# Kernel tuning notes

Measured on AMD Instinct MI355X. Metric: run time of the kernel, lower is better.

Reference implementation:

```python
import jax, jax.numpy as jnp
import numpy as np

TAU = 0.07
K = 50
EPS = 1e-8


def _flat_norm(x):
    # [B, C, H, W] -> [B*H*W, C], L2-normalized along C
    B, C = x.shape[0], x.shape[1]
    x = jnp.moveaxis(x, 1, -1).reshape(-1, C)
    n = jnp.linalg.norm(x, axis=-1, keepdims=True)
    return x / jnp.maximum(n, 1e-12)


def setup_inputs() -> dict:
    key = jax.random.key(0)
    ks = jax.random.split(key, 5)
    shp = (2, 128, 64, 64)
    lshp = (2, 4, 64, 64)
    return {
        "input": jax.random.normal(ks[0], shp, dtype=jnp.float32),
        "positive": jax.random.normal(ks[1], shp, dtype=jnp.float32),
        "negative": jax.random.normal(ks[2], shp, dtype=jnp.float32),
        "input_logits": jax.random.normal(ks[3], lshp, dtype=jnp.float32),
        "negative_logits": jax.random.normal(ks[4], lshp, dtype=jnp.float32),
    }


def reference(input, positive, negative, input_logits, negative_logits):
    norm_input = _flat_norm(input)        # [N, C]
    norm_positive = _flat_norm(positive)  # [N, C]
    norm_negative = _flat_norm(negative)  # [N, C]

    # check_input: multi-class logits branch (softmax over class dim, then max)
    in_probs = jax.nn.softmax(input_logits, axis=1)
    neg_probs = jax.nn.softmax(negative_logits, axis=1)
    seg_input = jnp.argmax(in_probs, axis=1).reshape(-1)       # [N] int
    seg_negative = jnp.argmax(neg_probs, axis=1).reshape(-1)   # [N] int
    negative_prob = jnp.max(neg_probs, axis=1).reshape(-1)     # [N] float

    # positive cosine similarity (unit vectors -> dot product)
    pos_sim = jnp.sum(norm_input * norm_positive, axis=-1)     # [N]

    # mask[i, j] = (seg_input[j] != seg_negative[i]) * negative_prob[i]
    diff = (seg_input[None, :] != seg_negative[:, None]).astype(jnp.float16)
    masked = diff.astype(jnp.float32) * negative_prob[:, None]  # [N, N]

    # top-k over dim=0 (negatives) for each input column j -> indices [N, K]
    _, idx = jax.lax.top_k(masked.T, K)                         # [N, K]
    sampled = norm_negative[idx]                                # [N, K, C]

    neg_sim = jnp.einsum('nkc,nc->nk', sampled, norm_input)     # [N, K]
    nominator = jnp.exp(pos_sim / TAU)                          # [N]
    denominator = jnp.sum(jnp.exp(neg_sim / TAU), axis=1) + nominator
    loss = -jnp.mean(jnp.log(nominator / (denominator + EPS)))

    alter_sim = jnp.einsum('nkc,nc->nk', sampled, norm_positive)
    alter_den = jnp.sum(jnp.exp(alter_sim / TAU), axis=1) + nominator
    alter_loss = -jnp.mean(jnp.log(nominator / (alter_den + EPS)))

    return loss + alter_loss
```

## Files before the change

kernel.cpp:

```cpp
#include <hip/hip_runtime.h>
#include <math.h>

#define TAU_INV (1.0f / 0.07f)
#define KSEL 50
#define KPAD 64
#define NPIX 8192
#define CCH 128
#define HWSZ 4096
#define NCLS 4
#define EPSL 1e-8f
#define NBINS 1026
#define PXT 32
#define SROW 132

__global__ void __launch_bounds__(1024) prep_kernel(
        const float* __restrict__ input, const float* __restrict__ positive,
        const float* __restrict__ negative,
        const float* __restrict__ ilog, const float* __restrict__ nlog,
        float* __restrict__ ni, float* __restrict__ np_,
        float* __restrict__ nnsel,
        int* __restrict__ perm, int* __restrict__ cnt,
        float* __restrict__ out) {
    __shared__ union {
        struct {
            float tile[CCH][65];
            float partial[4][64];
            float invn[64];
        } a;
        struct {
            unsigned hist[NBINS];
            unsigned coarse[33];
            unsigned long long cand[2048];
            unsigned wsum[16];
            int topk_l[KPAD];
            unsigned above_cnt, cand_cnt;
            int sB, sc0;
        } b;
    } sm;

    int t = threadIdx.x;
    int bid = blockIdx.x;

    if (bid >= NCLS) {
        int blk = bid - NCLS;
        int tensor = blk >> 7, chunk = blk & 127;
        const float* src = (tensor == 0) ? input : positive;
        float*       dst = (tensor == 0) ? ni    : np_;

        int n0 = chunk * 64;
        int b = n0 >> 12, hw0 = n0 & (HWSZ - 1);
        const float* base = src + (size_t)b * CCH * HWSZ + hw0;

        if (t < 256) {
            #pragma unroll
            for (int i = 0; i < 8; ++i) {
                int lin = t + i * 256;
                int cc = lin >> 4, hwq = (lin & 15) * 4;
                float4 v = *(const float4*)&base[(size_t)cc * HWSZ + hwq];
                sm.a.tile[cc][hwq + 0] = v.x; sm.a.tile[cc][hwq + 1] = v.y;
                sm.a.tile[cc][hwq + 2] = v.z; sm.a.tile[cc][hwq + 3] = v.w;
            }
        }
        __syncthreads();

        if (t < 256) {
            int nof = t & 63, part = t >> 6;
            float s = 0.f;
            #pragma unroll
            for (int j = 0; j < 32; ++j) {
                float v = sm.a.tile[part * 32 + j][nof];
                s += v * v;
            }
            sm.a.partial[part][nof] = s;
        }
        __syncthreads();
        if (t < 64) {
            float tot = sm.a.partial[0][t] + sm.a.partial[1][t] +
                        sm.a.partial[2][t] + sm.a.partial[3][t];
            sm.a.invn[t] = 1.0f / fmaxf(sqrtf(tot), 1e-12f);
        }
        __syncthreads();

        if (t < 256) {
            #pragma unroll
            for (int i = 0; i < 8; ++i) {
                int lin = t + i * 256;
                int nf = lin >> 5, cq = (lin & 31) * 4;
                float inv = sm.a.invn[nf];
                float4 o;
                o.x = sm.a.tile[cq + 0][nf] * inv;
                o.y = sm.a.tile[cq + 1][nf] * inv;
                o.z = sm.a.tile[cq + 2][nf] * inv;
                o.w = sm.a.tile[cq + 3][nf] * inv;
                *(float4*)&dst[(size_t)(n0 + nf) * CCH + cq] = o;
            }
        }
        return;
    }

    int c = bid;
    if (c == 0 && t == 0) out[0] = 0.0f;

    for (int i = t; i < NBINS; i += 1024) sm.b.hist[i] = 0;
    if (t < 33) sm.b.coarse[t] = 0;
    if (t == 0) { sm.b.above_cnt = 0; sm.b.cand_cnt = 0; }
    __syncthreads();

    unsigned keys[8];
    unsigned mask = 0u;
    #pragma unroll
    for (int s = 0; s < 2; ++s) {
        int i4 = (t * 2 + s) * 4;
        int b = i4 >> 12, hw = i4 & (HWSZ - 1);

        const float* pi = ilog + (size_t)b * NCLS * HWSZ + hw;
        float4 a0 = *(const float4*)&pi[0];
        float4 a1 = *(const float4*)&pi[HWSZ];
        float4 a2 = *(const float4*)&pi[2 * HWSZ];
        float4 a3 = *(const float4*)&pi[3 * HWSZ];
        const float* pn = nlog + (size_t)b * NCLS * HWSZ + hw;
        float4 b0 = *(const float4*)&pn[0];
        float4 b1 = *(const float4*)&pn[HWSZ];
        float4 b2 = *(const float4*)&pn[2 * HWSZ];
        float4 b3 = *(const float4*)&pn[3 * HWSZ];

        const float* A0 = (const float*)&a0; const float* A1 = (const float*)&a1;
        const float* A2 = (const float*)&a2; const float* A3 = (const float*)&a3;
        const float* B0 = (const float*)&b0; const float* B1 = (const float*)&b1;
        const float* B2 = (const float*)&b2; const float* B3 = (const float*)&b3;
        #pragma unroll
        for (int j = 0; j < 4; ++j) {
            float l0 = A0[j], l1 = A1[j], l2 = A2[j], l3 = A3[j];
            int bi = 0; float bv = l0;
            if (l1 > bv) { bv = l1; bi = 1; }
            if (l2 > bv) { bv = l2; bi = 2; }
            if (l3 > bv) { bv = l3; bi = 3; }
            if (bi == c) mask |= (1u << (s * 4 + j));

            float m0 = B0[j], m1 = B1[j], m2 = B2[j], m3 = B3[j];
            int ci = 0; float cv = m0;
            if (m1 > cv) { cv = m1; ci = 1; }
            if (m2 > cv) { cv = m2; ci = 2; }
            if (m3 > cv) { cv = m3; ci = 3; }
            float ssum = expf(m0 - cv) + expf(m1 - cv) + expf(m2 - cv) + expf(m3 - cv);
            float npv = 1.0f / ssum;

            float v = (ci != c) ? npv : 0.0f;
            unsigned key = __float_as_uint(v);
            keys[s * 4 + j] = key;
            int bin = (key < 0x3E800000u) ? 0 : (int)(1u + ((key - 0x3E800000u) >> 14));
            atomicAdd(&sm.b.hist[bin], 1u);
        }
    }

    {
        int cnt_t = __popc(mask);
        int lane = t & 63, wv = t >> 6;
        int x = cnt_t;
        #pragma unroll
        for (int off = 1; off < 64; off <<= 1) {
            int o = __shfl_up(x, off);
            if (lane >= off) x += o;
        }
        if (lane == 63) sm.b.wsum[wv] = (unsigned)x;
        __syncthreads();
        int base = x - cnt_t;
        for (int ww = 0; ww < wv; ++ww) base += (int)sm.b.wsum[ww];
        unsigned mm = mask;
        while (mm) {
            int bit = __ffs(mm) - 1; mm &= (mm - 1);
            perm[c * NPIX + base] = t * 8 + bit;
            ++base;
        }
        if (t == 0) {
            int tot = 0;
            for (int w2 = 0; w2 < 16; ++w2) tot += (int)sm.b.wsum[w2];
            cnt[c] = tot;
        }
    }

    for (int i = t; i < NBINS; i += 1024) atomicAdd(&sm.b.coarse[i >> 5], sm.b.hist[i]);
    __syncthreads();

    if (t == 0) {
        unsigned cum = 0; int j = 32;
        for (; j > 0; --j) {
            unsigned h = sm.b.coarse[j];
            if (cum + h >= KSEL) break;
            cum += h;
        }
        int hi = j * 32 + 31; if (hi > NBINS - 1) hi = NBINS - 1;
        int B = 0;
        for (int b = hi; b >= j * 32; --b) {
            unsigned h = sm.b.hist[b];
            if (cum + h >= KSEL) { B = b; break; }
            cum += h;
        }
        sm.b.sB = B; sm.b.sc0 = (int)cum;
    }
    __syncthreads();
    int B = sm.b.sB, c0 = sm.b.sc0;

    #pragma unroll
    for (int s = 0; s < 2; ++s) {
        #pragma unroll
        for (int j = 0; j < 4; ++j) {
            unsigned key = keys[s * 4 + j];
            int bin = (key < 0x3E800000u) ? 0 : (int)(1u + ((key - 0x3E800000u) >> 14));
            int i = t * 8 + s * 4 + j;
            if (bin > B) {
                unsigned pos = atomicAdd(&sm.b.above_cnt, 1u);
                sm.b.topk_l[pos] = i;
            } else if (bin == B) {
                unsigned jj = atomicAdd(&sm.b.cand_cnt, 1u);
                if (jj < 2048)
                    sm.b.cand[jj] = ((unsigned long long)key << 32) |
                                    (unsigned long long)(0xFFFFFFFFu - (unsigned)i);
            }
        }
    }
    __syncthreads();

    int m = KSEL - c0;
    int cb = (int)sm.b.cand_cnt; if (cb > 2048) cb = 2048;
    if (t < 64) {
        for (int r = 0; r < m; ++r) {
            unsigned long long best = 0;
            for (int j = t; j < cb; j += 64) {
                unsigned long long v = sm.b.cand[j];
                if (v > best) best = v;
            }
            #pragma unroll
            for (int off = 32; off; off >>= 1) {
                unsigned long long o = __shfl_xor(best, off);
                if (o > best) best = o;
            }
            if (t == 0) sm.b.topk_l[c0 + r] =
                (int)(0xFFFFFFFFu - (unsigned)(best & 0xFFFFFFFFull));
            for (int j = t; j < cb; j += 64)
                if (sm.b.cand[j] == best) sm.b.cand[j] = 0;
        }
    }
    __syncthreads();

    {
        int row = t >> 4;
        int ch0 = (t & 15) * 8;
        if (row < KSEL) {
            int px = sm.b.topk_l[row];
            int b = px >> 12, hw = px & (HWSZ - 1);
            const float* src = negative + (size_t)b * CCH * HWSZ + hw;
            float vals[8]; float ss = 0.f;
            #pragma unroll
            for (int k = 0; k < 8; ++k) {
                float v = src[(size_t)(ch0 + k) * HWSZ];
                vals[k] = v; ss += v * v;
            }
            ss += __shfl_xor(ss, 1);
            ss += __shfl_xor(ss, 2);
            ss += __shfl_xor(ss, 4);
            ss += __shfl_xor(ss, 8);
            float inv = 1.0f / fmaxf(sqrtf(ss), 1e-12f);
            float* dst = nnsel + (size_t)(c * KSEL + row) * CCH + ch0;
            #pragma unroll
            for (int k = 0; k < 8; ++k) dst[k] = vals[k] * inv;
        }
    }
}

__global__ void __launch_bounds__(256) loss_kernel(
        const float* __restrict__ ni, const float* __restrict__ npos,
        const float* __restrict__ nnsel,
        const int* __restrict__ perm, const int* __restrict__ cnt,
        float* __restrict__ out) {
    __shared__ float Sl[KPAD * SROW];
    __shared__ float Xl[PXT * SROW];
    __shared__ float Pl[PXT * SROW];
    __shared__ float bsum[4];

    int c = blockIdx.y;
    int count = cnt[c];
    int start = blockIdx.x * PXT;
    if (start >= count) return;
    int t = threadIdx.x;

    {
        int row = t >> 2;
        int ch0 = (t & 3) * 32;
        float* dst = &Sl[row * SROW + ch0];
        if (row < KSEL) {
            const float* src = nnsel + (size_t)(c * KSEL + row) * CCH + ch0;
            #pragma unroll
            for (int i = 0; i < 8; ++i)
                ((float4*)dst)[i] = ((const float4*)src)[i];
        } else {
            float4 z = make_float4(0.f, 0.f, 0.f, 0.f);
            #pragma unroll
            for (int i = 0; i < 8; ++i)
                ((float4*)dst)[i] = z;
        }
    }
    {
        int row = t >> 3;
        int slot = start + row;
        int px = perm[c * NPIX + ((slot < count) ? slot : start)];
        int ch0 = (t & 7) * 16;
        const float* sx = ni + (size_t)px * CCH + ch0;
        const float* sp = npos + (size_t)px * CCH + ch0;
        float* dx = &Xl[row * SROW + ch0];
        float* dp = &Pl[row * SROW + ch0];
        #pragma unroll
        for (int i = 0; i < 4; ++i) {
            ((float4*)dx)[i] = ((const float4*)sx)[i];
            ((float4*)dp)[i] = ((const float4*)sp)[i];
        }
    }
    __syncthreads();

    int ktid = t & 7, pxid = t >> 3;
    float acc_i[8] = {0.f, 0.f, 0.f, 0.f, 0.f, 0.f, 0.f, 0.f};
    float acc_p[8] = {0.f, 0.f, 0.f, 0.f, 0.f, 0.f, 0.f, 0.f};
    float ps = 0.f;
    const float* Xr = &Xl[pxid * SROW];
    const float* Pr = &Pl[pxid * SROW];

    #pragma unroll 2
    for (int ch = 0; ch < CCH; ch += 4) {
        float4 xv = *(const float4*)&Xr[ch];
        float4 pv = *(const float4*)&Pr[ch];
        ps += xv.x * pv.x + xv.y * pv.y + xv.z * pv.z + xv.w * pv.w;
        #pragma unroll
        for (int r = 0; r < 8; ++r) {
            float4 sv = *(const float4*)&Sl[(ktid + r * 8) * SROW + ch];
            acc_i[r] += sv.x * xv.x + sv.y * xv.y + sv.z * xv.z + sv.w * xv.w;
            acc_p[r] += sv.x * pv.x + sv.y * pv.y + sv.z * pv.z + sv.w * pv.w;
        }
    }

    float si = 0.f, spp = 0.f;
    #pragma unroll
    for (int r = 0; r < 8; ++r) {
        si  += expf(acc_i[r] * TAU_INV);
        spp += expf(acc_p[r] * TAU_INV);
    }
    #pragma unroll
    for (int off = 1; off < 8; off <<= 1) {
        si  += __shfl_xor(si, off);
        spp += __shfl_xor(spp, off);
    }

    float v = 0.f;
    if (ktid == 0 && (start + pxid) < count) {
        si  -= (float)(KPAD - KSEL);
        spp -= (float)(KPAD - KSEL);
        float nom = expf(ps * TAU_INV);
        float li = -logf(nom / (si + nom + EPSL));
        float lp = -logf(nom / (spp + nom + EPSL));
        v = (li + lp) * (1.0f / (float)NPIX);
    }
    v += __shfl_xor(v, 8);
    v += __shfl_xor(v, 16);
    v += __shfl_xor(v, 32);
    int w = t >> 6;
    if ((t & 63) == 0) bsum[w] = v;
    __syncthreads();
    if (t == 0) atomicAdd(out, bsum[0] + bsum[1] + bsum[2] + bsum[3]);
}

extern "C" void kernel_launch(void* const* d_in, const int* in_sizes, int n_in,
                              void* d_out, int out_size, void* d_ws, size_t ws_size,
                              hipStream_t stream) {
    const float* input      = (const float*)d_in[0];
    const float* positive   = (const float*)d_in[1];
    const float* negative   = (const float*)d_in[2];
    const float* in_logits  = (const float*)d_in[3];
    const float* neg_logits = (const float*)d_in[4];
    float* out = (float*)d_out;

    float* ws    = (float*)d_ws;
    float* ni    = ws;
    float* np_   = ws + 1048576;
    float* nnsel = ws + 2097152;
    int*   cnt   = (int*)(ws + 2097152 + 32768);
    int*   perm  = cnt + 64;

    prep_kernel<<<256 + NCLS, 1024, 0, stream>>>(input, positive, negative,
                                                 in_logits, neg_logits,
                                                 ni, np_, nnsel, perm, cnt, out);
    dim3 lgrid(NPIX / PXT, NCLS);
    loss_kernel<<<lgrid, 256, 0, stream>>>(ni, np_, nnsel, perm, cnt, out);
}
```

Baseline: 105.6 us.

## Use all threads in normalize prep and register-block two pixels per thread in loss

New measurement: 106.6 us. About the same (+0.9%).

```diff
diff --git a/kernel.cpp b/kernel.cpp
--- a/kernel.cpp
+++ b/kernel.cpp
@@ -24,7 +24,7 @@
     __shared__ union {
         struct {
             float tile[CCH][65];
-            float partial[4][64];
+            float partial[16][64];
             float invn[64];
         } a;
         struct {
@@ -51,49 +51,46 @@
         int b = n0 >> 12, hw0 = n0 & (HWSZ - 1);
         const float* base = src + (size_t)b * CCH * HWSZ + hw0;
 
-        if (t < 256) {
-            #pragma unroll
-            for (int i = 0; i < 8; ++i) {
-                int lin = t + i * 256;
-                int cc = lin >> 4, hwq = (lin & 15) * 4;
-                float4 v = *(const float4*)&base[(size_t)cc * HWSZ + hwq];
-                sm.a.tile[cc][hwq + 0] = v.x; sm.a.tile[cc][hwq + 1] = v.y;
-                sm.a.tile[cc][hwq + 2] = v.z; sm.a.tile[cc][hwq + 3] = v.w;
-            }
+        #pragma unroll
+        for (int i = 0; i < 2; ++i) {
+            int lin = t + i * 1024;
+            int cc = lin >> 4, hwq = (lin & 15) * 4;
+            float4 v = *(const float4*)&base[(size_t)cc * HWSZ + hwq];
+            sm.a.tile[cc][hwq + 0] = v.x; sm.a.tile[cc][hwq + 1] = v.y;
+            sm.a.tile[cc][hwq + 2] = v.z; sm.a.tile[cc][hwq + 3] = v.w;
         }
         __syncthreads();
 
-        if (t < 256) {
+        {
             int nof = t & 63, part = t >> 6;
             float s = 0.f;
             #pragma unroll
-            for (int j = 0; j < 32; ++j) {
-                float v = sm.a.tile[part * 32 + j][nof];
+            for (int j = 0; j < 8; ++j) {
+                float v = sm.a.tile[part * 8 + j][nof];
                 s += v * v;
             }
             sm.a.partial[part][nof] = s;
         }
         __syncthreads();
         if (t < 64) {
-            float tot = sm.a.partial[0][t] + sm.a.partial[1][t] +
-                        sm.a.partial[2][t] + sm.a.partial[3][t];
+            float tot = 0.f;
+            #pragma unroll
+            for (int p = 0; p < 16; ++p) tot += sm.a.partial[p][t];
             sm.a.invn[t] = 1.0f / fmaxf(sqrtf(tot), 1e-12f);
         }
         __syncthreads();
 
-        if (t < 256) {
-            #pragma unroll
-            for (int i = 0; i < 8; ++i) {
-                int lin = t + i * 256;
-                int nf = lin >> 5, cq = (lin & 31) * 4;
-                float inv = sm.a.invn[nf];
-                float4 o;
-                o.x = sm.a.tile[cq + 0][nf] * inv;
-                o.y = sm.a.tile[cq + 1][nf] * inv;
-                o.z = sm.a.tile[cq + 2][nf] * inv;
-                o.w = sm.a.tile[cq + 3][nf] * inv;
-                *(float4*)&dst[(size_t)(n0 + nf) * CCH + cq] = o;
-            }
+        #pragma unroll
+        for (int i = 0; i < 2; ++i) {
+            int lin = t + i * 1024;
+            int nf = lin >> 5, cq = (lin & 31) * 4;
+            float inv = sm.a.invn[nf];
+            float4 o;
+            o.x = sm.a.tile[cq + 0][nf] * inv;
+            o.y = sm.a.tile[cq + 1][nf] * inv;
+            o.z = sm.a.tile[cq + 2][nf] * inv;
+            o.w = sm.a.tile[cq + 3][nf] * inv;
+            *(float4*)&dst[(size_t)(n0 + nf) * CCH + cq] = o;
         }
         return;
     }
@@ -317,48 +314,78 @@
     }
     __syncthreads();
 
-    int ktid = t & 7, pxid = t >> 3;
-    float acc_i[8] = {0.f, 0.f, 0.f, 0.f, 0.f, 0.f, 0.f, 0.f};
-    float acc_p[8] = {0.f, 0.f, 0.f, 0.f, 0.f, 0.f, 0.f, 0.f};
-    float ps = 0.f;
-    const float* Xr = &Xl[pxid * SROW];
-    const float* Pr = &Pl[pxid * SROW];
+    int ktid = t & 7, chh = (t >> 3) & 1, pxid = t >> 4;
+    float acc_i0[8] = {0.f,0.f,0.f,0.f,0.f,0.f,0.f,0.f};
+    float acc_p0[8] = {0.f,0.f,0.f,0.f,0.f,0.f,0.f,0.f};
+    float acc_i1[8] = {0.f,0.f,0.f,0.f,0.f,0.f,0.f,0.f};
+    float acc_p1[8] = {0.f,0.f,0.f,0.f,0.f,0.f,0.f,0.f};
+    float ps0 = 0.f, ps1 = 0.f;
+    const float* Xr0 = &Xl[pxid * SROW + chh * 64];
+    const float* Pr0 = &Pl[pxid * SROW + chh * 64];
+    const float* Xr1 = &Xl[(pxid + 16) * SROW + chh * 64];
+    const float* Pr1 = &Pl[(pxid + 16) * SROW + chh * 64];
+    const float* Sb  = &Sl[ktid * SROW + chh * 64];
 
     #pragma unroll 2
-    for (int ch = 0; ch < CCH; ch += 4) {
-        float4 xv = *(const float4*)&Xr[ch];
-        float4 pv = *(const float4*)&Pr[ch];
-        ps += xv.x * pv.x + xv.y * pv.y + xv.z * pv.z + xv.w * pv.w;
+    for (int ch = 0; ch < 64; ch += 4) {
+        float4 xv0 = *(const float4*)&Xr0[ch];
+        float4 pv0 = *(const float4*)&Pr0[ch];
+        float4 xv1 = *(const float4*)&Xr1[ch];
+        float4 pv1 = *(const float4*)&Pr1[ch];
+        ps0 += xv0.x * pv0.x + xv0.y * pv0.y + xv0.z * pv0.z + xv0.w * pv0.w;
+        ps1 += xv1.x * pv1.x + xv1.y * pv1.y + xv1.z * pv1.z + xv1.w * pv1.w;
         #pragma unroll
         for (int r = 0; r < 8; ++r) {
-            float4 sv = *(const float4*)&Sl[(ktid + r * 8) * SROW + ch];
-            acc_i[r] += sv.x * xv.x + sv.y * xv.y + sv.z * xv.z + sv.w * xv.w;
-            acc_p[r] += sv.x * pv.x + sv.y * pv.y + sv.z * pv.z + sv.w * pv.w;
-        }
-    }
-
-    float si = 0.f, spp = 0.f;
+            float4 sv = *(const float4*)&Sb[r * 8 * SROW + ch];
+            acc_i0[r] += sv.x * xv0.x + sv.y * xv0.y + sv.z * xv0.z + sv.w * xv0.w;
+            acc_p0[r] += sv.x * pv0.x + sv.y * pv0.y + sv.z * pv0.z + sv.w * pv0.w;
+            acc_i1[r] += sv.x * xv1.x + sv.y * xv1.y + sv.z * xv1.z + sv.w * xv1.w;
+            acc_p1[r] += sv.x * pv1.x + sv.y * pv1.y + sv.z * pv1.z + sv.w * pv1.w;
+        }
+    }
+
     #pragma unroll
     for (int r = 0; r < 8; ++r) {
-        si  += expf(acc_i[r] * TAU_INV);
-        spp += expf(acc_p[r] * TAU_INV);
+        acc_i0[r] += __shfl_xor(acc_i0[r], 8);
+        acc_p0[r] += __shfl_xor(acc_p0[r], 8);
+        acc_i1[r] += __shfl_xor(acc_i1[r], 8);
+        acc_p1[r] += __shfl_xor(acc_p1[r], 8);
+    }
+    ps0 += __shfl_xor(ps0, 8);
+    ps1 += __shfl_xor(ps1, 8);
+
+    float si0 = 0.f, sp0 = 0.f, si1 = 0.f, sp1 = 0.f;
+    #pragma unroll
+    for (int r = 0; r < 8; ++r) {
+        si0 += expf(acc_i0[r] * TAU_INV);
+        sp0 += expf(acc_p0[r] * TAU_INV);
+        si1 += expf(acc_i1[r] * TAU_INV);
+        sp1 += expf(acc_p1[r] * TAU_INV);
     }
     #pragma unroll
     for (int off = 1; off < 8; off <<= 1) {
-        si  += __shfl_xor(si, off);
-        spp += __shfl_xor(spp, off);
+        si0 += __shfl_xor(si0, off);
+        sp0 += __shfl_xor(sp0, off);
+        si1 += __shfl_xor(si1, off);
+        sp1 += __shfl_xor(sp1, off);
     }
 
     float v = 0.f;
-    if (ktid == 0 && (start + pxid) < count) {
-        si  -= (float)(KPAD - KSEL);
-        spp -= (float)(KPAD - KSEL);
-        float nom = expf(ps * TAU_INV);
-        float li = -logf(nom / (si + nom + EPSL));
-        float lp = -logf(nom / (spp + nom + EPSL));
-        v = (li + lp) * (1.0f / (float)NPIX);
-    }
-    v += __shfl_xor(v, 8);
+    if ((t & 15) == 0) {
+        if (start + pxid < count) {
+            float s  = si0 - (float)(KPAD - KSEL);
+            float sp = sp0 - (float)(KPAD - KSEL);
+            float nom = expf(ps0 * TAU_INV);
+            v += -logf(nom / (s + nom + EPSL)) - logf(nom / (sp + nom + EPSL));
+        }
+        if (start + pxid + 16 < count) {
+            float s  = si1 - (float)(KPAD - KSEL);
+            float sp = sp1 - (float)(KPAD - KSEL);
+            float nom = expf(ps1 * TAU_INV);
+            v += -logf(nom / (s + nom + EPSL)) - logf(nom / (sp + nom + EPSL));
+        }
+        v *= (1.0f / (float)NPIX);
+    }
     v += __shfl_xor(v, 16);
     v += __shfl_xor(v, 32);
     int w = t >> 6;
```

## Replace per-class pixel permutation with in-block class lookup over all four negative sets

Applied to the files above, without the earlier changes.

Result: no change. 104.8 us (-0.8%).

```diff
diff --git a/kernel.cpp b/kernel.cpp
--- a/kernel.cpp
+++ b/kernel.cpp
@@ -3,7 +3,7 @@
 
 #define TAU_INV (1.0f / 0.07f)
 #define KSEL 50
-#define KPAD 64
+#define KROW 56
 #define NPIX 8192
 #define CCH 128
 #define HWSZ 4096
@@ -12,6 +12,7 @@
 #define NBINS 1026
 #define PXT 32
 #define SROW 132
+#define SCLS (KROW * SROW + 8)
 
 __global__ void __launch_bounds__(1024) prep_kernel(
         const float* __restrict__ input, const float* __restrict__ positive,
@@ -19,20 +20,18 @@
         const float* __restrict__ ilog, const float* __restrict__ nlog,
         float* __restrict__ ni, float* __restrict__ np_,
         float* __restrict__ nnsel,
-        int* __restrict__ perm, int* __restrict__ cnt,
         float* __restrict__ out) {
     __shared__ union {
         struct {
             float tile[CCH][65];
-            float partial[4][64];
+            float partial[16][64];
             float invn[64];
         } a;
         struct {
             unsigned hist[NBINS];
             unsigned coarse[33];
             unsigned long long cand[2048];
-            unsigned wsum[16];
-            int topk_l[KPAD];
+            int topk_l[64];
             unsigned above_cnt, cand_cnt;
             int sB, sc0;
         } b;
@@ -51,49 +50,46 @@
         int b = n0 >> 12, hw0 = n0 & (HWSZ - 1);
         const float* base = src + (size_t)b * CCH * HWSZ + hw0;
 
-        if (t < 256) {
-            #pragma unroll
-            for (int i = 0; i < 8; ++i) {
-                int lin = t + i * 256;
-                int cc = lin >> 4, hwq = (lin & 15) * 4;
-                float4 v = *(const float4*)&base[(size_t)cc * HWSZ + hwq];
-                sm.a.tile[cc][hwq + 0] = v.x; sm.a.tile[cc][hwq + 1] = v.y;
-                sm.a.tile[cc][hwq + 2] = v.z; sm.a.tile[cc][hwq + 3] = v.w;
-            }
+        #pragma unroll
+        for (int i = 0; i < 2; ++i) {
+            int lin = t + i * 1024;
+            int cc = lin >> 4, hwq = (lin & 15) * 4;
+            float4 v = *(const float4*)&base[(size_t)cc * HWSZ + hwq];
+            sm.a.tile[cc][hwq + 0] = v.x; sm.a.tile[cc][hwq + 1] = v.y;
+            sm.a.tile[cc][hwq + 2] = v.z; sm.a.tile[cc][hwq + 3] = v.w;
         }
         __syncthreads();
 
-        if (t < 256) {
+        {
             int nof = t & 63, part = t >> 6;
             float s = 0.f;
             #pragma unroll
-            for (int j = 0; j < 32; ++j) {
-                float v = sm.a.tile[part * 32 + j][nof];
+            for (int j = 0; j < 8; ++j) {
+                float v = sm.a.tile[part * 8 + j][nof];
                 s += v * v;
             }
             sm.a.partial[part][nof] = s;
         }
         __syncthreads();
         if (t < 64) {
-            float tot = sm.a.partial[0][t] + sm.a.partial[1][t] +
-                        sm.a.partial[2][t] + sm.a.partial[3][t];
+            float tot = 0.f;
+            #pragma unroll
+            for (int p = 0; p < 16; ++p) tot += sm.a.partial[p][t];
             sm.a.invn[t] = 1.0f / fmaxf(sqrtf(tot), 1e-12f);
         }
         __syncthreads();
 
-        if (t < 256) {
-            #pragma unroll
-            for (int i = 0; i < 8; ++i) {
-                int lin = t + i * 256;
-                int nf = lin >> 5, cq = (lin & 31) * 4;
-                float inv = sm.a.invn[nf];
-                float4 o;
-                o.x = sm.a.tile[cq + 0][nf] * inv;
-                o.y = sm.a.tile[cq + 1][nf] * inv;
-                o.z = sm.a.tile[cq + 2][nf] * inv;
-                o.w = sm.a.tile[cq + 3][nf] * inv;
-                *(float4*)&dst[(size_t)(n0 + nf) * CCH + cq] = o;
-            }
+        #pragma unroll
+        for (int i = 0; i < 2; ++i) {
+            int lin = t + i * 1024;
+            int nf = lin >> 5, cq = (lin & 31) * 4;
+            float inv = sm.a.invn[nf];
+            float4 o;
+            o.x = sm.a.tile[cq + 0][nf] * inv;
+            o.y = sm.a.tile[cq + 1][nf] * inv;
+            o.z = sm.a.tile[cq + 2][nf] * inv;
+            o.w = sm.a.tile[cq + 3][nf] * inv;
+            *(float4*)&dst[(size_t)(n0 + nf) * CCH + cq] = o;
         }
         return;
     }
@@ -107,36 +103,21 @@
     __syncthreads();
 
     unsigned keys[8];
-    unsigned mask = 0u;
     #pragma unroll
     for (int s = 0; s < 2; ++s) {
         int i4 = (t * 2 + s) * 4;
         int b = i4 >> 12, hw = i4 & (HWSZ - 1);
 
-        const float* pi = ilog + (size_t)b * NCLS * HWSZ + hw;
-        float4 a0 = *(const float4*)&pi[0];
-        float4 a1 = *(const float4*)&pi[HWSZ];
-        float4 a2 = *(const float4*)&pi[2 * HWSZ];
-        float4 a3 = *(const float4*)&pi[3 * HWSZ];
         const float* pn = nlog + (size_t)b * NCLS * HWSZ + hw;
         float4 b0 = *(const float4*)&pn[0];
         float4 b1 = *(const float4*)&pn[HWSZ];
         float4 b2 = *(const float4*)&pn[2 * HWSZ];
         float4 b3 = *(const float4*)&pn[3 * HWSZ];
 
-        const float* A0 = (const float*)&a0; const float* A1 = (const float*)&a1;
-        const float* A2 = (const float*)&a2; const float* A3 = (const float*)&a3;
         const float* B0 = (const float*)&b0; const float* B1 = (const float*)&b1;
         const float* B2 = (const float*)&b2; const float* B3 = (const float*)&b3;
         #pragma unroll
         for (int j = 0; j < 4; ++j) {
-            float l0 = A0[j], l1 = A1[j], l2 = A2[j], l3 = A3[j];
-            int bi = 0; float bv = l0;
-            if (l1 > bv) { bv = l1; bi = 1; }
-            if (l2 > bv) { bv = l2; bi = 2; }
-            if (l3 > bv) { bv = l3; bi = 3; }
-            if (bi == c) mask |= (1u << (s * 4 + j));
-
             float m0 = B0[j], m1 = B1[j], m2 = B2[j], m3 = B3[j];
             int ci = 0; float cv = m0;
             if (m1 > cv) { cv = m1; ci = 1; }
@@ -152,32 +133,7 @@
             atomicAdd(&sm.b.hist[bin], 1u);
         }
     }
-
-    {
-        int cnt_t = __popc(mask);
-        int lane = t & 63, wv = t >> 6;
-        int x = cnt_t;
-        #pragma unroll
-        for (int off = 1; off < 64; off <<= 1) {
-            int o = __shfl_up(x, off);
-            if (lane >= off) x += o;
-        }
-        if (lane == 63) sm.b.wsum[wv] = (unsigned)x;
-        __syncthreads();
-        int base = x - cnt_t;
-        for (int ww = 0; ww < wv; ++ww) base += (int)sm.b.wsum[ww];
-        unsigned mm = mask;
-        while (mm) {
-            int bit = __ffs(mm) - 1; mm &= (mm - 1);
-            perm[c * NPIX + base] = t * 8 + bit;
-            ++base;
-        }
-        if (t == 0) {
-            int tot = 0;
-            for (int w2 = 0; w2 < 16; ++w2) tot += (int)sm.b.wsum[w2];
-            cnt[c] = tot;
-        }
-    }
+    __syncthreads();
 
     for (int i = t; i < NBINS; i += 1024) atomicAdd(&sm.b.coarse[i >> 5], sm.b.hist[i]);
     __syncthreads();
@@ -261,49 +217,52 @@
             ss += __shfl_xor(ss, 4);
             ss += __shfl_xor(ss, 8);
             float inv = 1.0f / fmaxf(sqrtf(ss), 1e-12f);
-            float* dst = nnsel + (size_t)(c * KSEL + row) * CCH + ch0;
+            float* dst = nnsel + (size_t)(c * KROW + row) * CCH + ch0;
             #pragma unroll
             for (int k = 0; k < 8; ++k) dst[k] = vals[k] * inv;
+        } else if (row < KROW) {
+            float* dst = nnsel + (size_t)(c * KROW + row) * CCH + ch0;
+            #pragma unroll
+            for (int k = 0; k < 8; ++k) dst[k] = 0.f;
         }
     }
 }
 
 __global__ void __launch_bounds__(256) loss_kernel(
         const float* __restrict__ ni, const float* __restrict__ npos,
-        const float* __restrict__ nnsel,
-        const int* __restrict__ perm, const int* __restrict__ cnt,
+        const float* __restrict__ nnsel, const float* __restrict__ ilog,
         float* __restrict__ out) {
-    __shared__ float Sl[KPAD * SROW];
+    __shared__ float Sl[NCLS * SCLS];
     __shared__ float Xl[PXT * SROW];
     __shared__ float Pl[PXT * SROW];
+    __shared__ int   clsL[PXT];
     __shared__ float bsum[4];
 
-    int c = blockIdx.y;
-    int count = cnt[c];
+    int t = threadIdx.x;
     int start = blockIdx.x * PXT;
-    if (start >= count) return;
-    int t = threadIdx.x;
-
-    {
-        int row = t >> 2;
-        int ch0 = (t & 3) * 32;
-        float* dst = &Sl[row * SROW + ch0];
-        if (row < KSEL) {
-            const float* src = nnsel + (size_t)(c * KSEL + row) * CCH + ch0;
-            #pragma unroll
-            for (int i = 0; i < 8; ++i)
-                ((float4*)dst)[i] = ((const float4*)src)[i];
-        } else {
-            float4 z = make_float4(0.f, 0.f, 0.f, 0.f);
-            #pragma unroll
-            for (int i = 0; i < 8; ++i)
-                ((float4*)dst)[i] = z;
-        }
+
+    for (int i = t; i < NCLS * KROW * 32; i += 256) {
+        int rowq = i >> 5;
+        int q = i & 31;
+        int cc = rowq / KROW;
+        int rr = rowq - cc * KROW;
+        float4 v = *(const float4*)&nnsel[(size_t)rowq * CCH + q * 4];
+        *(float4*)&Sl[cc * SCLS + rr * SROW + q * 4] = v;
+    }
+    if (t < PXT) {
+        int px = start + t;
+        int b = px >> 12, hw = px & (HWSZ - 1);
+        const float* pi = ilog + (size_t)b * NCLS * HWSZ + hw;
+        float l0 = pi[0], l1 = pi[HWSZ], l2 = pi[2 * HWSZ], l3 = pi[3 * HWSZ];
+        int bi = 0; float bv = l0;
+        if (l1 > bv) { bv = l1; bi = 1; }
+        if (l2 > bv) { bv = l2; bi = 2; }
+        if (l3 > bv) { bv = l3; bi = 3; }
+        clsL[t] = bi;
     }
     {
         int row = t >> 3;
-        int slot = start + row;
-        int px = perm[c * NPIX + ((slot < count) ? slot : start)];
+        int px = start + row;
         int ch0 = (t & 7) * 16;
         const float* sx = ni + (size_t)px * CCH + ch0;
         const float* sp = npos + (size_t)px * CCH + ch0;
@@ -318,11 +277,14 @@
     __syncthreads();
 
     int ktid = t & 7, pxid = t >> 3;
-    float acc_i[8] = {0.f, 0.f, 0.f, 0.f, 0.f, 0.f, 0.f, 0.f};
-    float acc_p[8] = {0.f, 0.f, 0.f, 0.f, 0.f, 0.f, 0.f, 0.f};
-    float ps = 0.f;
+    int cls = clsL[pxid];
+    const float* Sb = &Sl[cls * SCLS + ktid * SROW];
     const float* Xr = &Xl[pxid * SROW];
     const float* Pr = &Pl[pxid * SROW];
+
+    float acc_i[7] = {0.f, 0.f, 0.f, 0.f, 0.f, 0.f, 0.f};
+    float acc_p[7] = {0.f, 0.f, 0.f, 0.f, 0.f, 0.f, 0.f};
+    float ps = 0.f;
 
     #pragma unroll 2
     for (int ch = 0; ch < CCH; ch += 4) {
@@ -330,8 +292,8 @@
         float4 pv = *(const float4*)&Pr[ch];
         ps += xv.x * pv.x + xv.y * pv.y + xv.z * pv.z + xv.w * pv.w;
         #pragma unroll
-        for (int r = 0; r < 8; ++r) {
-            float4 sv = *(const float4*)&Sl[(ktid + r * 8) * SROW + ch];
+        for (int r = 0; r < 7; ++r) {
+            float4 sv = *(const float4*)&Sb[r * 8 * SROW + ch];
             acc_i[r] += sv.x * xv.x + sv.y * xv.y + sv.z * xv.z + sv.w * xv.w;
             acc_p[r] += sv.x * pv.x + sv.y * pv.y + sv.z * pv.z + sv.w * pv.w;
         }
@@ -339,7 +301,7 @@
 
     float si = 0.f, spp = 0.f;
     #pragma unroll
-    for (int r = 0; r < 8; ++r) {
+    for (int r = 0; r < 7; ++r) {
         si  += expf(acc_i[r] * TAU_INV);
         spp += expf(acc_p[r] * TAU_INV);
     }
@@ -350,9 +312,9 @@
     }
 
     float v = 0.f;
-    if (ktid == 0 && (start + pxid) < count) {
-        si  -= (float)(KPAD - KSEL);
-        spp -= (float)(KPAD - KSEL);
+    if (ktid == 0) {
+        si  -= (float)(KROW - KSEL);
+        spp -= (float)(KROW - KSEL);
         float nom = expf(ps * TAU_INV);
         float li = -logf(nom / (si + nom + EPSL));
         float lp = -logf(nom / (spp + nom + EPSL));
@@ -381,12 +343,9 @@
     float* ni    = ws;
     float* np_   = ws + 1048576;
     float* nnsel = ws + 2097152;
-    int*   cnt   = (int*)(ws + 2097152 + 32768);
-    int*   perm  = cnt + 64;
 
     prep_kernel<<<256 + NCLS, 1024, 0, stream>>>(input, positive, negative,
                                                  in_logits, neg_logits,
-                                                 ni, np_, nnsel, perm, cnt, out);
-    dim3 lgrid(NPIX / PXT, NCLS);
-    loss_kernel<<<lgrid, 256, 0, stream>>>(ni, np_, nnsel, perm, cnt, out);
+                                                 ni, np_, nnsel, out);
+    loss_kernel<<<NPIX / PXT, 256, 0, stream>>>(ni, np_, nnsel, in_logits, out);
 }
```
